# Kernel optimization log

Measured on AMD Instinct MI355X. Metric: run time of the kernel, lower is better.

## Reference

```python
import jax, jax.numpy as jnp
import numpy as np

GATE_INIT_BIAS = -0.6931471805599453  # -log(2)

def mish(x):
    return x * jnp.tanh(jax.nn.softplus(x))

def setup_inputs() -> dict:
    key = jax.random.key(0)
    ks = jax.random.split(key, 24)
    B = 262144
    x = jax.random.normal(ks[0], (B, 18), dtype=jnp.float32)
    band = jax.random.randint(ks[1], (B,), 0, 9).astype(jnp.float32)
    x = x.at[:, 17].set(band)
    def lin(k, fan_in, shape):
        bound = 1.0 / np.sqrt(fan_in)
        return jax.random.uniform(k, shape, jnp.float32, -bound, bound)
    inp = {
        'x': x,
        # trunk: 15->512->256 (Mish)
        'tw1': lin(ks[2], 15, (15, 512)),  'tb1': lin(ks[3], 15, (512,)),
        'tw2': lin(ks[4], 512, (512, 256)), 'tb2': lin(ks[5], 512, (256,)),
        # 9 band heads: 256->128->1, stacked on leading axis
        'hw1': lin(ks[6], 256, (9, 256, 128)), 'hb1': lin(ks[7], 256, (9, 128)),
        'hw2': lin(ks[8], 128, (9, 128)),      'hb2': lin(ks[9], 128, (9,)),
        # sun scaler head 256->64->1 (final layer zero weight, bias = gate_init_bias)
        'sw1': lin(ks[10], 256, (256, 64)), 'sb1': lin(ks[11], 256, (64,)),
        'sw2': jnp.zeros((64, 1), jnp.float32), 'sb2': jnp.full((1,), GATE_INIT_BIAS, jnp.float32),
        # storm scaler head
        'stw1': lin(ks[12], 256, (256, 64)), 'stb1': lin(ks[13], 256, (64,)),
        'stw2': jnp.zeros((64, 1), jnp.float32), 'stb2': jnp.full((1,), GATE_INIT_BIAS, jnp.float32),
        # monotonic sidecars: 1->8->1, softplus-positivized weights
        'sun_w1': lin(ks[14], 1, (1, 8)),  'sun_b1': lin(ks[15], 1, (8,)),
        'sun_w2': lin(ks[16], 8, (8, 1)),  'sun_b2': lin(ks[17], 8, (1,)),
        'storm_w1': lin(ks[18], 1, (1, 8)), 'storm_b1': lin(ks[19], 1, (8,)),
        'storm_w2': lin(ks[20], 8, (8, 1)), 'storm_b2': lin(ks[21], 8, (1,)),
    }
    return inp

def monotonic_mlp(v, w1, b1, w2, b2):
    # MonotonicMLP: positivity via softplus on weights, tanh hidden activation
    h = jnp.tanh(v @ jax.nn.softplus(w1) + b1)
    return h @ jax.nn.softplus(w2) + b2  # [B,1]

def reference(x, tw1, tb1, tw2, tb2, hw1, hb1, hw2, hb2,
              sw1, sb1, sw2, sb2, stw1, stb1, stw2, stb2,
              sun_w1, sun_b1, sun_w2, sun_b2,
              storm_w1, storm_b1, storm_w2, storm_b2):
    x_deep = x[:, :15]
    x_sfi = x[:, 15:16]
    x_kp = x[:, 16:17]
    band = x[:, 17].astype(jnp.int32)  # [B]

    # trunk
    t = mish(mish(x_deep @ tw1 + tb1) @ tw2 + tb2)  # [B,256]

    # all 9 band heads densely (faithful to original), then gather
    hh = mish(jnp.einsum('bd,kdh->bkh', t, hw1) + hb1)       # [B,9,128]
    all_heads = jnp.einsum('bkh,kh->bk', hh, hw2) + hb2      # [B,9]
    base_snr = jnp.take_along_axis(all_heads, band[:, None], axis=1)  # [B,1]

    sun_logit = mish(t @ sw1 + sb1) @ sw2 + sb2      # [B,1]
    storm_logit = mish(t @ stw1 + stb1) @ stw2 + stb2
    sun_gate = jax.nn.sigmoid(sun_logit)
    storm_gate = jax.nn.sigmoid(storm_logit)

    return base_snr + sun_gate * monotonic_mlp(x_sfi, sun_w1, sun_b1, sun_w2, sun_b2) \
                    + storm_gate * monotonic_mlp(x_kp, storm_w1, storm_b1, storm_w2, storm_b2)
```

## Files before the change

### kernel.cpp

```cpp
#include <hip/hip_runtime.h>
#include <cstdint>

typedef unsigned short u16;
typedef unsigned char u8;
typedef __attribute__((ext_vector_type(8))) __bf16 bf16x8;
typedef __attribute__((ext_vector_type(4))) float f32x4;

#define MFMA16(a, b, c) __builtin_amdgcn_mfma_f32_16x16x32_bf16((a), (b), (c), 0, 0, 0)

__device__ __forceinline__ u16 f2b(float f) {
    union { float f; unsigned u; } v; v.f = f;
    unsigned r = v.u + 0x7fffu + ((v.u >> 16) & 1u);
    return (u16)(r >> 16);
}
__device__ __forceinline__ u16 f2b_hw(float f) {
    union { __bf16 h; u16 u; } cv; cv.h = (__bf16)f; return cv.u;
}
__device__ __forceinline__ float b2f(u16 h) {
    union { unsigned u; float f; } v; v.u = ((unsigned)h) << 16; return v.f;
}
__device__ __forceinline__ float fast_rcp(float x) { return __builtin_amdgcn_rcpf(x); }
__device__ __forceinline__ float mish_f(float x) {
    float e = __expf(fminf(x, 40.0f));
    float u = 1.0f + e;
    float u2 = u * u;
    return x * (u2 - 1.0f) * fast_rcp(u2 + 1.0f);
}
__device__ __forceinline__ float tanh_f(float y) {
    float e = __expf(2.0f * y);
    return 1.0f - 2.0f * fast_rcp(e + 1.0f);
}
__device__ __forceinline__ float sigmoid_f(float y) {
    return fast_rcp(1.0f + __expf(-y));
}
__device__ __forceinline__ float splus(float w) { return log1pf(__expf(w)); }

template <int CTRL>
__device__ __forceinline__ float dpp_add(float v) {
    union { float f; int i; } s, p;
    s.f = v;
    p.i = __builtin_amdgcn_update_dpp(0, s.i, CTRL, 0xf, 0xf, true);
    return v + p.f;
}
__device__ __forceinline__ float row16_sum(float v) {
    v = dpp_add<0xB1>(v);
    v = dpp_add<0x4E>(v);
    v = dpp_add<0x141>(v);
    v = dpp_add<0x140>(v);
    return v;
}

#define WS_PERM      0u
#define WS_GSC       1048576u
#define WS_GOFF      1048640u
#define WS_BBAND     1048704u
#define WS_BSTART    1065152u
#define WS_BNROWS    1081600u
#define WS_SP        1098048u
#define WS_GPART     1098176u
#define WS_BANDS     1116608u
#define WS_W1P       1378752u
#define WS_W2F       1411520u
#define WS_HW1F      1673664u
#define WS_SWF       2263488u
#define WS_STWF      2296256u
#define WS_NEEDED    2329024u

#define PACK_BLOCKS  512


__global__ void k_pack(const float* __restrict__ x, int B,
                       const float* __restrict__ tw1, const float* __restrict__ tw2,
                       const float* __restrict__ hw1,
                       const float* __restrict__ sw1, const float* __restrict__ stw1,
                       const float* __restrict__ sun_w1, const float* __restrict__ sun_w2,
                       const float* __restrict__ storm_w1, const float* __restrict__ storm_w2,
                       u16* __restrict__ W1p, u16* __restrict__ W2f, u16* __restrict__ HWf,
                       u16* __restrict__ SWf, u16* __restrict__ STWf,
                       float* __restrict__ sp, int* __restrict__ gpart,
                       u8* __restrict__ bands)
{
    __shared__ int h[9];
    int ltid = threadIdx.x;
    int tid = blockIdx.x * blockDim.x + ltid;
    if (ltid < 9) h[ltid] = 0;
    __syncthreads();
    for (int i = tid; i < B; i += PACK_BLOCKS * 256) {
        int b = (int)x[i * 18 + 17];
        bands[i] = (u8)b;
        atomicAdd(&h[b], 1);
    }

    if (tid < 32) {
        const float* srcs[4] = { sun_w1, sun_w2, storm_w1, storm_w2 };
        float w = srcs[tid >> 3][tid & 7];
        sp[tid] = splus(w);
    }
    const int total = 16384 + 131072 + 294912 + 16384 + 16384;
    for (int i = tid; i < total; i += PACK_BLOCKS * 256) {
        int idx = i;
        if (idx < 16384) {
            int n = idx >> 5, k = idx & 31;
            W1p[idx] = (k < 15) ? f2b(tw1[k * 512 + n]) : (u16)0;
        } else if ((idx -= 16384) < 131072) {
            int tile = idx >> 9, within = idx & 511;
            int lane = within >> 3, j = within & 7;
            int nt = tile >> 4, kb = tile & 15;
            int n = nt * 16 + (lane & 15);
            int k = kb * 32 + (lane >> 4) * 8 + j;
            W2f[idx] = f2b(tw2[k * 256 + n]);
        } else if ((idx -= 131072) < 294912) {
            int g = idx >> 15, r = idx & 32767;
            int tile = r >> 9, within = r & 511;
            int lane = within >> 3, j = within & 7;
            int nt = tile >> 3, kb = tile & 7;
            int n = nt * 16 + (lane & 15);
            int k = kb * 32 + (lane >> 4) * 8 + j;
            HWf[idx] = f2b(hw1[(g * 256 + k) * 128 + n]);
        } else if ((idx -= 294912) < 16384) {
            int tile = idx >> 9, within = idx & 511;
            int lane = within >> 3, j = within & 7;
            int nt = tile >> 3, kb = tile & 7;
            int n = nt * 16 + (lane & 15);
            int k = kb * 32 + (lane >> 4) * 8 + j;
            SWf[idx] = f2b(sw1[k * 64 + n]);
        } else {
            idx -= 16384;
            int tile = idx >> 9, within = idx & 511;
            int lane = within >> 3, j = within & 7;
            int nt = tile >> 3, kb = tile & 7;
            int n = nt * 16 + (lane & 15);
            int k = kb * 32 + (lane >> 4) * 8 + j;
            STWf[idx] = f2b(stw1[k * 64 + n]);
        }
    }
    __syncthreads();
    if (ltid < 9) gpart[blockIdx.x * 9 + ltid] = h[ltid];
}

__global__ void k_table(const int* __restrict__ gpart, int* __restrict__ goff,
                        int* __restrict__ gsc, int* __restrict__ blk_band,
                        int* __restrict__ blk_start, int* __restrict__ blk_nrows, int nblk_max)
{
    __shared__ int s_goff[10], s_bstart[10], s_cnt[9];
    int tid = threadIdx.x;
    if (tid < 9) {
        int s = 0;
        for (int b = 0; b < PACK_BLOCKS; ++b) s += gpart[b * 9 + tid];
        s_cnt[tid] = s;
    }
    __syncthreads();
    if (tid == 0) {
        int off = 0, boff = 0;
        for (int g = 0; g < 9; ++g) {
            s_goff[g] = off; goff[g] = off;
            s_bstart[g] = boff;
            off += s_cnt[g];
            boff += (s_cnt[g] + 63) >> 6;
        }
        s_goff[9] = off; goff[9] = off;
        s_bstart[9] = boff;
        for (int g = 0; g < 9; ++g) gsc[g] = 0;
    }
    __syncthreads();
    for (int b = tid; b < nblk_max; b += blockDim.x) {
        int band = -1, loc = 0;
        for (int g = 0; g < 9; ++g)
            if (b >= s_bstart[g] && b < s_bstart[g + 1]) { band = g; loc = b - s_bstart[g]; }
        blk_band[b] = band;
        if (band >= 0) {
            blk_start[b] = s_goff[band] + loc * 64;
            int rem = s_cnt[band] - loc * 64;
            blk_nrows[b] = rem < 64 ? rem : 64;
        } else { blk_start[b] = 0; blk_nrows[b] = 0; }
    }
}

__global__ void k_scatter(const u8* __restrict__ bands, const int* __restrict__ goff,
                          int* __restrict__ gsc, int* __restrict__ perm, int B)
{
    __shared__ int wcnt[4][9];
    __shared__ int wpre[4][9];
    __shared__ int gbase[9];
    int tid = threadIdx.x;
    int lane = tid & 63, wave = tid >> 6;
    int i = blockIdx.x * blockDim.x + tid;
    int band = -1, rank = 0;
    if (i < B) band = (int)bands[i];
    for (int k = 0; k < 9; ++k) {
        unsigned long long m = __ballot(band == k);
        if (band == k) rank = __popcll(m & ((1ull << lane) - 1ull));
        if (lane == 0) wcnt[wave][k] = __popcll(m);
    }
    __syncthreads();
    if (tid < 9) {
        int k = tid, run = 0;
        for (int w = 0; w < 4; ++w) { wpre[w][k] = run; run += wcnt[w][k]; }
        gbase[k] = (run > 0) ? atomicAdd(&gsc[k], run) : 0;
    }
    __syncthreads();
    if (i < B && band >= 0) {
        int pos = goff[band] + gbase[band] + wpre[wave][band] + rank;
        perm[pos] = i;
    }
}

__global__ __launch_bounds__(512, 4) void k_main(
                       const float* __restrict__ x,
                       const int* __restrict__ perm,
                       const int* __restrict__ blk_band,
                       const int* __restrict__ blk_start,
                       const int* __restrict__ blk_nrows,
                       const u16* __restrict__ W1p, const u16* __restrict__ W2f,
                       const u16* __restrict__ HWf,
                       const u16* __restrict__ SWf, const u16* __restrict__ STWf,
                       const float* __restrict__ tb1, const float* __restrict__ tb2,
                       const float* __restrict__ hb1, const float* __restrict__ hw2,
                       const float* __restrict__ hb2,
                       const float* __restrict__ sb1, const float* __restrict__ sw2,
                       const float* __restrict__ sb2,
                       const float* __restrict__ stb1, const float* __restrict__ stw2,
                       const float* __restrict__ stb2,
                       const float* __restrict__ sp,
                       const float* __restrict__ sun_b1, const float* __restrict__ sun_b2,
                       const float* __restrict__ storm_b1, const float* __restrict__ storm_b2,
                       float* __restrict__ out)
{
    int bb = blk_band[blockIdx.x];
    if (bb < 0) return;
    int rstart = blk_start[blockIdx.x];
    int nrows  = blk_nrows[blockIdx.x];

    __shared__ union {
        u16 xA[64][32];
        float red[16][64];
    } su;
    __shared__ int rowsL[64];
    __shared__ float sfiL[64], kpL[64];
    __shared__ u16 buf[2][64][136];

    int tid = threadIdx.x;
    int lane = tid & 63, wave = tid >> 6;
    int quad = lane >> 4, l15 = lane & 15;

    if (tid < 64) {
        int r = rstart + (tid < nrows ? tid : 0);
        rowsL[tid] = perm[r];
    }
    for (int i = tid; i < 64 * 32; i += 512) ((u16*)su.xA)[i] = 0;
    __syncthreads();
    for (int i = tid; i < 64 * 18; i += 512) {
        int r = i / 18, c = i - r * 18;
        float v = x[rowsL[r] * 18 + c];
        if (c < 15) su.xA[r][c] = f2b_hw(v);
        else if (c == 15) sfiL[r] = v;
        else if (c == 16) kpL[r] = v;
    }
    __syncthreads();

    bf16x8 ax[4];
#pragma unroll
    for (int mt = 0; mt < 4; ++mt)
        ax[mt] = *(const bf16x8*)&su.xA[mt * 16 + l15][quad * 8];

    f32x4 acc2[2][4] = {};

    for (int c = 0; c < 4; ++c) {
        f32x4 acc1[4] = {};
        {
            int ncol = c * 128 + wave * 16 + l15;
            bf16x8 bw = *(const bf16x8*)&W1p[ncol * 32 + quad * 8];
#pragma unroll
            for (int mt = 0; mt < 4; ++mt)
                acc1[mt] = MFMA16(ax[mt], bw, acc1[mt]);
        }
        u16 (*bufc)[136] = buf[c & 1];
        {
            int ccol = wave * 16 + l15;
            float bias = tb1[c * 128 + ccol];
#pragma unroll
            for (int mt = 0; mt < 4; ++mt)
#pragma unroll
                for (int r = 0; r < 4; ++r)
                    bufc[mt * 16 + quad * 4 + r][ccol] = f2b_hw(mish_f(acc1[mt][r] + bias));
        }
        __syncthreads();
        for (int ks = 0; ks < 4; ++ks) {
            bf16x8 a2[4];
#pragma unroll
            for (int mt = 0; mt < 4; ++mt)
                a2[mt] = *(const bf16x8*)&bufc[mt * 16 + l15][ks * 32 + quad * 8];
            int kb = c * 4 + ks;
#pragma unroll
            for (int ntl = 0; ntl < 2; ++ntl) {
                int nt = wave * 2 + ntl;
                bf16x8 bw = *(const bf16x8*)&W2f[((nt * 16 + kb) << 9) + lane * 8];
#pragma unroll
                for (int mt = 0; mt < 4; ++mt)
                    acc2[ntl][mt] = MFMA16(a2[mt], bw, acc2[ntl][mt]);
            }
        }
    }
    __syncthreads();

    u16 (*tmat)[264] = (u16(*)[264])buf;
#pragma unroll
    for (int ntl = 0; ntl < 2; ++ntl) {
        int col = wave * 32 + ntl * 16 + l15;
        float bias = tb2[col];
#pragma unroll
        for (int mt = 0; mt < 4; ++mt)
#pragma unroll
            for (int r = 0; r < 4; ++r)
                tmat[mt * 16 + quad * 4 + r][col] = f2b_hw(mish_f(acc2[ntl][mt][r] + bias));
    }
    __syncthreads();

    f32x4 acch[4] = {}, accg[4] = {};
    const u16* Hw = HWf + bb * 32768;
    const u16* Gw = (wave < 4) ? SWf : STWf;
    int gnt = wave & 3;
    for (int kb = 0; kb < 8; ++kb) {
        bf16x8 a3[4];
#pragma unroll
        for (int mt = 0; mt < 4; ++mt)
            a3[mt] = *(const bf16x8*)&tmat[mt * 16 + l15][kb * 32 + quad * 8];
        bf16x8 bh = *(const bf16x8*)&Hw[((wave * 8 + kb) << 9) + lane * 8];
        bf16x8 bg = *(const bf16x8*)&Gw[((gnt * 8 + kb) << 9) + lane * 8];
#pragma unroll
        for (int mt = 0; mt < 4; ++mt) {
            acch[mt] = MFMA16(a3[mt], bh, acch[mt]);
            accg[mt] = MFMA16(a3[mt], bg, accg[mt]);
        }
    }

    float hsum[4][4];
    {
        int col = wave * 16 + l15;
        float hb = hb1[bb * 128 + col];
        float wv = hw2[bb * 128 + col];
#pragma unroll
        for (int mt = 0; mt < 4; ++mt)
#pragma unroll
            for (int r = 0; r < 4; ++r)
                hsum[mt][r] = mish_f(acch[mt][r] + hb) * wv;
    }
    float gsum[4][4];
    {
        int n = gnt * 16 + l15;
        float gb = (wave < 4) ? sb1[n] : stb1[n];
        float gw = (wave < 4) ? sw2[n] : stw2[n];
#pragma unroll
        for (int mt = 0; mt < 4; ++mt)
#pragma unroll
            for (int r = 0; r < 4; ++r)
                gsum[mt][r] = mish_f(accg[mt][r] + gb) * gw;
    }
#pragma unroll
    for (int mt = 0; mt < 4; ++mt)
#pragma unroll
        for (int r = 0; r < 4; ++r) {
            hsum[mt][r] = row16_sum(hsum[mt][r]);
            gsum[mt][r] = row16_sum(gsum[mt][r]);
        }
    if (l15 == 0)
#pragma unroll
        for (int mt = 0; mt < 4; ++mt)
#pragma unroll
            for (int r = 0; r < 4; ++r) {
                int row = mt * 16 + quad * 4 + r;
                su.red[wave][row] = hsum[mt][r];
                su.red[8 + wave][row] = gsum[mt][r];
            }
    __syncthreads();

    if (tid < 64 && tid < nrows) {
        int row = tid;
        float head = hb2[bb];
#pragma unroll
        for (int w = 0; w < 8; ++w) head += su.red[w][row];
        float sl = sb2[0], tl = stb2[0];
#pragma unroll
        for (int w = 0; w < 4; ++w) { sl += su.red[8 + w][row]; tl += su.red[12 + w][row]; }
        float sg = sigmoid_f(sl);
        float tg = sigmoid_f(tl);
        float v1 = sfiL[row], v2 = kpL[row];
        float sun_val = sun_b2[0], storm_val = storm_b2[0];
#pragma unroll
        for (int j = 0; j < 8; ++j) {
            sun_val   += tanh_f(v1 * sp[j]      + sun_b1[j])   * sp[8 + j];
            storm_val += tanh_f(v2 * sp[16 + j] + storm_b1[j]) * sp[24 + j];
        }
        out[rowsL[row]] = head + sg * sun_val + tg * storm_val;
    }
}

__global__ __launch_bounds__(64) void k_simple(
    const float* __restrict__ x,
    const float* __restrict__ tw1, const float* __restrict__ tb1,
    const float* __restrict__ tw2, const float* __restrict__ tb2,
    const float* __restrict__ hw1, const float* __restrict__ hb1,
    const float* __restrict__ hw2, const float* __restrict__ hb2,
    const float* __restrict__ sw1, const float* __restrict__ sb1,
    const float* __restrict__ sw2, const float* __restrict__ sb2,
    const float* __restrict__ stw1, const float* __restrict__ stb1,
    const float* __restrict__ stw2, const float* __restrict__ stb2,
    const float* __restrict__ sun_w1, const float* __restrict__ sun_b1,
    const float* __restrict__ sun_w2, const float* __restrict__ sun_b2,
    const float* __restrict__ storm_w1, const float* __restrict__ storm_b1,
    const float* __restrict__ storm_w2, const float* __restrict__ storm_b2,
    float* __restrict__ out)
{
    __shared__ u16 t_lds[256 * 64];

    const int lane = threadIdx.x;
    const int r = blockIdx.x * 64 + lane;

    float xr[15];
#pragma unroll
    for (int k = 0; k < 15; ++k) xr[k] = x[r * 18 + k];
    const float sfi = x[r * 18 + 15];
    const float kp  = x[r * 18 + 16];
    const int band  = (int)x[r * 18 + 17];

    for (int tc = 0; tc < 4; ++tc) {
        float acc[64];
#pragma unroll
        for (int j = 0; j < 64; ++j) acc[j] = 0.0f;
        for (int n = 0; n < 512; ++n) {
            float p = tb1[n];
#pragma unroll
            for (int k = 0; k < 15; ++k) p += xr[k] * tw1[k * 512 + n];
            const float a1n = mish_f(p);
            const float* w2 = &tw2[n * 256 + tc * 64];
#pragma unroll
            for (int j = 0; j < 64; ++j) acc[j] += a1n * w2[j];
        }
#pragma unroll
        for (int j = 0; j < 64; ++j)
            t_lds[(tc * 64 + j) * 64 + lane] = f2b(mish_f(acc[j] + tb2[tc * 64 + j]));
    }
    __syncthreads();

    float head_val = 0.0f;
    for (int g = 0; g < 9; ++g) {
        float hs = 0.0f;
        for (int hc = 0; hc < 2; ++hc) {
            float pre[64];
#pragma unroll
            for (int j = 0; j < 64; ++j) pre[j] = 0.0f;
            for (int d = 0; d < 256; ++d) {
                const float td = b2f(t_lds[d * 64 + lane]);
                const float* wv = &hw1[g * 32768 + d * 128 + hc * 64];
#pragma unroll
                for (int j = 0; j < 64; ++j) pre[j] += td * wv[j];
            }
#pragma unroll
            for (int j = 0; j < 64; ++j) {
                const int h = hc * 64 + j;
                hs += mish_f(pre[j] + hb1[g * 128 + h]) * hw2[g * 128 + h];
            }
        }
        head_val += (band == g) ? (hs + hb2[g]) : 0.0f;
    }

    float pre_s[64], pre_t[64];
#pragma unroll
    for (int j = 0; j < 64; ++j) { pre_s[j] = 0.0f; pre_t[j] = 0.0f; }
    for (int d = 0; d < 256; ++d) {
        const float td = b2f(t_lds[d * 64 + lane]);
        const float* ws1 = &sw1[d * 64];
        const float* wt1 = &stw1[d * 64];
#pragma unroll
        for (int j = 0; j < 64; ++j) {
            pre_s[j] += td * ws1[j];
            pre_t[j] += td * wt1[j];
        }
    }
    float ls = sb2[0], lt = stb2[0];
#pragma unroll
    for (int j = 0; j < 64; ++j) {
        ls += mish_f(pre_s[j] + sb1[j]) * sw2[j];
        lt += mish_f(pre_t[j] + stb1[j]) * stw2[j];
    }
    const float sg = sigmoid_f(ls);
    const float tg = sigmoid_f(lt);

    float sun_val = sun_b2[0], storm_val = storm_b2[0];
#pragma unroll
    for (int j = 0; j < 8; ++j) {
        sun_val   += tanh_f(sfi * splus(sun_w1[j])  + sun_b1[j])   * splus(sun_w2[j]);
        storm_val += tanh_f(kp * splus(storm_w1[j]) + storm_b1[j]) * splus(storm_w2[j]);
    }

    out[r] = head_val + sg * sun_val + tg * storm_val;
}

extern "C" void kernel_launch(void* const* d_in, const int* in_sizes, int n_in,
                              void* d_out, int out_size, void* d_ws, size_t ws_size,
                              hipStream_t stream) {
    (void)n_in; (void)out_size;
    const float* x        = (const float*)d_in[0];
    const float* tw1      = (const float*)d_in[1];
    const float* tb1      = (const float*)d_in[2];
    const float* tw2      = (const float*)d_in[3];
    const float* tb2      = (const float*)d_in[4];
    const float* hw1      = (const float*)d_in[5];
    const float* hb1      = (const float*)d_in[6];
    const float* hw2      = (const float*)d_in[7];
    const float* hb2      = (const float*)d_in[8];
    const float* sw1      = (const float*)d_in[9];
    const float* sb1      = (const float*)d_in[10];
    const float* sw2      = (const float*)d_in[11];
    const float* sb2      = (const float*)d_in[12];
    const float* stw1     = (const float*)d_in[13];
    const float* stb1     = (const float*)d_in[14];
    const float* stw2     = (const float*)d_in[15];
    const float* stb2     = (const float*)d_in[16];
    const float* sun_w1   = (const float*)d_in[17];
    const float* sun_b1   = (const float*)d_in[18];
    const float* sun_w2   = (const float*)d_in[19];
    const float* sun_b2   = (const float*)d_in[20];
    const float* storm_w1 = (const float*)d_in[21];
    const float* storm_b1 = (const float*)d_in[22];
    const float* storm_w2 = (const float*)d_in[23];
    const float* storm_b2 = (const float*)d_in[24];

    const int B = in_sizes[0] / 18;

    if (ws_size < (size_t)WS_NEEDED) {
        k_simple<<<B / 64, 64, 0, stream>>>(x, tw1, tb1, tw2, tb2, hw1, hb1, hw2, hb2,
                                            sw1, sb1, sw2, sb2, stw1, stb1, stw2, stb2,
                                            sun_w1, sun_b1, sun_w2, sun_b2,
                                            storm_w1, storm_b1, storm_w2, storm_b2,
                                            (float*)d_out);
        return;
    }

    char* ws = (char*)d_ws;
    int*   perm      = (int*)(ws + WS_PERM);
    int*   gsc       = (int*)(ws + WS_GSC);
    int*   goff      = (int*)(ws + WS_GOFF);
    int*   blk_band  = (int*)(ws + WS_BBAND);
    int*   blk_start = (int*)(ws + WS_BSTART);
    int*   blk_nrows = (int*)(ws + WS_BNROWS);
    float* sp        = (float*)(ws + WS_SP);
    int*   gpart     = (int*)(ws + WS_GPART);
    u8*    bands     = (u8*)(ws + WS_BANDS);
    u16*   W1p       = (u16*)(ws + WS_W1P);
    u16*   W2f       = (u16*)(ws + WS_W2F);
    u16*   HWf       = (u16*)(ws + WS_HW1F);
    u16*   SWf       = (u16*)(ws + WS_SWF);
    u16*   STWf      = (u16*)(ws + WS_STWF);

    int nblk = B / 64 + 16;

    k_pack<<<PACK_BLOCKS, 256, 0, stream>>>(x, B, tw1, tw2, hw1, sw1, stw1,
                                            sun_w1, sun_w2, storm_w1, storm_w2,
                                            W1p, W2f, HWf, SWf, STWf, sp, gpart, bands);
    k_table<<<1, 256, 0, stream>>>(gpart, goff, gsc, blk_band, blk_start, blk_nrows, nblk);
    k_scatter<<<(B + 255) / 256, 256, 0, stream>>>(bands, goff, gsc, perm, B);
    k_main<<<nblk, 512, 0, stream>>>(x, perm, blk_band, blk_start, blk_nrows,
                                     W1p, W2f, HWf, SWf, STWf,
                                     tb1, tb2, hb1, hw2, hb2,
                                     sb1, sw2, sb2, stb1, stw2, stb2,
                                     sp, sun_b1, sun_b2, storm_b1, storm_b2,
                                     (float*)d_out);
}
```

Measured before the change: 326.7 us.

## Make band scatter deterministic via per-chunk prefix table; simplify mish algebra

The band histogram in k_pack now covers contiguous chunks, one per block. k_table builds a per-chunk exclusive prefix table, and k_scatter uses it to place rows directly in stable order with no global atomics, using 512-thread blocks that match the chunks. Mish is also rewritten as x*p/(p+2) with p=s(s+2), which drops a few arithmetic ops per activation. The scatter now assumes B is divisible by PACK_BLOCKS*512-sized chunks, and k_table does a serial 512-step prefix loop per band.

```diff
diff --git a/kernel.cpp b/kernel.cpp
--- a/kernel.cpp
+++ b/kernel.cpp
@@ -21,10 +21,9 @@
 }
 __device__ __forceinline__ float fast_rcp(float x) { return __builtin_amdgcn_rcpf(x); }
 __device__ __forceinline__ float mish_f(float x) {
-    float e = __expf(fminf(x, 40.0f));
-    float u = 1.0f + e;
-    float u2 = u * u;
-    return x * (u2 - 1.0f) * fast_rcp(u2 + 1.0f);
+    float s = __expf(fminf(x, 40.0f));
+    float p = s * (s + 2.0f);
+    return x * p * fast_rcp(p + 2.0f);
 }
 __device__ __forceinline__ float tanh_f(float y) {
     float e = __expf(2.0f * y);
@@ -51,20 +50,20 @@
 }
 
 #define WS_PERM      0u
-#define WS_GSC       1048576u
-#define WS_GOFF      1048640u
-#define WS_BBAND     1048704u
-#define WS_BSTART    1065152u
-#define WS_BNROWS    1081600u
-#define WS_SP        1098048u
-#define WS_GPART     1098176u
-#define WS_BANDS     1116608u
-#define WS_W1P       1378752u
-#define WS_W2F       1411520u
-#define WS_HW1F      1673664u
-#define WS_SWF       2263488u
-#define WS_STWF      2296256u
-#define WS_NEEDED    2329024u
+#define WS_GOFF      1048576u
+#define WS_BBAND     1048640u
+#define WS_BSTART    1065088u
+#define WS_BNROWS    1081536u
+#define WS_SP        1097984u
+#define WS_GPART     1098112u
+#define WS_CPRE      1116544u
+#define WS_BANDS     1134976u
+#define WS_W1P       1397120u
+#define WS_W2F       1429888u
+#define WS_HW1F      1692032u
+#define WS_SWF       2281856u
+#define WS_STWF      2314624u
+#define WS_NEEDED    2347392u
 
 #define PACK_BLOCKS  512
 
@@ -85,9 +84,12 @@
     int tid = blockIdx.x * blockDim.x + ltid;
     if (ltid < 9) h[ltid] = 0;
     __syncthreads();
-    for (int i = tid; i < B; i += PACK_BLOCKS * 256) {
-        int b = (int)x[i * 18 + 17];
-        bands[i] = (u8)b;
+    const int CH = B / PACK_BLOCKS;
+    const int base = blockIdx.x * CH;
+    for (int i = ltid; i < CH; i += 256) {
+        int r = base + i;
+        int b = (int)x[r * 18 + 17];
+        bands[r] = (u8)b;
         atomicAdd(&h[b], 1);
     }
 
@@ -138,31 +140,37 @@
     if (ltid < 9) gpart[blockIdx.x * 9 + ltid] = h[ltid];
 }
 
-__global__ void k_table(const int* __restrict__ gpart, int* __restrict__ goff,
-                        int* __restrict__ gsc, int* __restrict__ blk_band,
+__global__ void k_table(const int* __restrict__ gpart, int* __restrict__ cpre,
+                        int* __restrict__ blk_band,
                         int* __restrict__ blk_start, int* __restrict__ blk_nrows, int nblk_max)
 {
     __shared__ int s_goff[10], s_bstart[10], s_cnt[9];
     int tid = threadIdx.x;
     if (tid < 9) {
         int s = 0;
-        for (int b = 0; b < PACK_BLOCKS; ++b) s += gpart[b * 9 + tid];
+        for (int c = 0; c < PACK_BLOCKS; ++c) s += gpart[c * 9 + tid];
         s_cnt[tid] = s;
     }
     __syncthreads();
     if (tid == 0) {
         int off = 0, boff = 0;
         for (int g = 0; g < 9; ++g) {
-            s_goff[g] = off; goff[g] = off;
+            s_goff[g] = off;
             s_bstart[g] = boff;
             off += s_cnt[g];
             boff += (s_cnt[g] + 63) >> 6;
         }
-        s_goff[9] = off; goff[9] = off;
+        s_goff[9] = off;
         s_bstart[9] = boff;
-        for (int g = 0; g < 9; ++g) gsc[g] = 0;
-    }
-    __syncthreads();
+    }
+    __syncthreads();
+    if (tid < 9) {
+        int run = s_goff[tid];
+        for (int c = 0; c < PACK_BLOCKS; ++c) {
+            cpre[c * 9 + tid] = run;
+            run += gpart[c * 9 + tid];
+        }
+    }
     for (int b = tid; b < nblk_max; b += blockDim.x) {
         int band = -1, loc = 0;
         for (int g = 0; g < 9; ++g)
@@ -176,15 +184,15 @@
     }
 }
 
-__global__ void k_scatter(const u8* __restrict__ bands, const int* __restrict__ goff,
-                          int* __restrict__ gsc, int* __restrict__ perm, int B)
+__global__ __launch_bounds__(512) void k_scatter(const u8* __restrict__ bands,
+                                                 const int* __restrict__ cpre,
+                                                 int* __restrict__ perm, int B)
 {
-    __shared__ int wcnt[4][9];
-    __shared__ int wpre[4][9];
-    __shared__ int gbase[9];
+    __shared__ int wcnt[8][9];
+    __shared__ int wpre[8][9];
     int tid = threadIdx.x;
     int lane = tid & 63, wave = tid >> 6;
-    int i = blockIdx.x * blockDim.x + tid;
+    int i = blockIdx.x * 512 + tid;
     int band = -1, rank = 0;
     if (i < B) band = (int)bands[i];
     for (int k = 0; k < 9; ++k) {
@@ -194,15 +202,12 @@
     }
     __syncthreads();
     if (tid < 9) {
-        int k = tid, run = 0;
-        for (int w = 0; w < 4; ++w) { wpre[w][k] = run; run += wcnt[w][k]; }
-        gbase[k] = (run > 0) ? atomicAdd(&gsc[k], run) : 0;
-    }
-    __syncthreads();
-    if (i < B && band >= 0) {
-        int pos = goff[band] + gbase[band] + wpre[wave][band] + rank;
-        perm[pos] = i;
-    }
+        int run = 0;
+        for (int w = 0; w < 8; ++w) { wpre[w][tid] = run; run += wcnt[w][tid]; }
+    }
+    __syncthreads();
+    if (i < B && band >= 0)
+        perm[cpre[blockIdx.x * 9 + band] + wpre[wave][band] + rank] = i;
 }
 
 __global__ __launch_bounds__(512, 4) void k_main(
@@ -539,13 +544,12 @@
 
     char* ws = (char*)d_ws;
     int*   perm      = (int*)(ws + WS_PERM);
-    int*   gsc       = (int*)(ws + WS_GSC);
-    int*   goff      = (int*)(ws + WS_GOFF);
     int*   blk_band  = (int*)(ws + WS_BBAND);
     int*   blk_start = (int*)(ws + WS_BSTART);
     int*   blk_nrows = (int*)(ws + WS_BNROWS);
     float* sp        = (float*)(ws + WS_SP);
     int*   gpart     = (int*)(ws + WS_GPART);
+    int*   cpre      = (int*)(ws + WS_CPRE);
     u8*    bands     = (u8*)(ws + WS_BANDS);
     u16*   W1p       = (u16*)(ws + WS_W1P);
     u16*   W2f       = (u16*)(ws + WS_W2F);
@@ -558,8 +562,8 @@
     k_pack<<<PACK_BLOCKS, 256, 0, stream>>>(x, B, tw1, tw2, hw1, sw1, stw1,
                                             sun_w1, sun_w2, storm_w1, storm_w2,
                                             W1p, W2f, HWf, SWf, STWf, sp, gpart, bands);
-    k_table<<<1, 256, 0, stream>>>(gpart, goff, gsc, blk_band, blk_start, blk_nrows, nblk);
-    k_scatter<<<(B + 255) / 256, 256, 0, stream>>>(bands, goff, gsc, perm, B);
+    k_table<<<1, 256, 0, stream>>>(gpart, cpre, blk_band, blk_start, blk_nrows, nblk);
+    k_scatter<<<PACK_BLOCKS, 512, 0, stream>>>(bands, cpre, perm, B);
     k_main<<<nblk, 512, 0, stream>>>(x, perm, blk_band, blk_start, blk_nrows,
                                      W1p, W2f, HWf, SWf, STWf,
                                      tb1, tb2, hb1, hw2, hb2,
```

Result: no change. 322.0 us (-1.4%).
